# Performance work log

Measured on AMD Instinct MI355X. Metric: run time of the kernel, lower is better.

## Reference

```python
import jax, jax.numpy as jnp
import numpy as np

B, F, D = 1024, 39, 16
HIDDEN = [128, 128, 128]


def _cin(x, Ws, bs):
    # x: (B, F0, D) stacked field embeddings
    F0 = x.shape[1]
    h = x  # hidden_nn_layers[-1], shape (B, Fk, D)
    outs = []
    n = len(Ws)
    for i, (W, b) in enumerate(zip(Ws, bs)):
        L = W.shape[-1]
        Fk = h.shape[1]
        Wr = W.reshape(F0, Fk, L)  # conv1d kernel [1, F0*Fk, L] -> (F0, Fk, L)
        # per-embedding-dim field outer product: (B, F0, Fk, D)
        z = jnp.einsum('bfd,bgd->bfgd', x, h)
        # pointwise conv over D + bias + relu -> (B, L, D)
        cur = jax.nn.relu(jnp.einsum('bfgd,fgl->bld', z, Wr) + b[None, :, None])
        if i != n - 1:
            h = cur[:, : L // 2]          # next_hidden
            direct = cur[:, L // 2 :]     # direct_connect
        else:
            direct = cur
        outs.append(direct)
    # concat over field axis, sum over embedding dim -> (B, sum_direct)
    return jnp.concatenate(outs, axis=1).sum(-1)


def setup_inputs() -> dict:
    key = jax.random.key(0)
    ks = jax.random.split(key, 8)
    x = jax.random.normal(ks[0], (B, F, D), dtype=jnp.float32)
    field_nums = [F]
    Ws, bs = [], []
    for i, L in enumerate(HIDDEN):
        fan_in = field_nums[0] * field_nums[-1]
        lim = np.sqrt(6.0 / fan_in)  # he_uniform
        Ws.append(jax.random.uniform(ks[1 + i], (fan_in, L), jnp.float32, -lim, lim))
        bs.append(jnp.zeros((L,), jnp.float32))
        field_nums.append(L // 2)
    return {"x": x, "W0": Ws[0], "W1": Ws[1], "W2": Ws[2],
            "b0": bs[0], "b1": bs[1], "b2": bs[2]}


def reference(x, W0, W1, W2, b0, b1, b2):
    return _cin(x, [W0, W1, W2], [b0, b1, b2])
```

## Files before the change

kernel.cpp:

```cpp
#include <hip/hip_runtime.h>


#define NF     39
#define LCH    128
#define NLAYER 3
#define NFT    (NLAYER * NF)

typedef __bf16        bf16x8 __attribute__((ext_vector_type(8)));
typedef unsigned int  uint4v __attribute__((ext_vector_type(4)));
typedef float         f32x4  __attribute__((ext_vector_type(4)));

__device__ __forceinline__ unsigned short f2bf_rne(float f) {
    unsigned u = __float_as_uint(f);
    u += 0x7fffu + ((u >> 16) & 1u);
    return (unsigned short)(u >> 16);
}

__global__ void cin_prep(const float* __restrict__ W0,
                         const float* __restrict__ W1,
                         const float* __restrict__ W2,
                         unsigned short* __restrict__ wt)
{
    const int t = blockIdx.x * blockDim.x + threadIdx.x;
    if (t >= NFT * 1024) return;
    const int n  = t & 127;
    const int q  = (t >> 7) & 3;
    const int ks = (t >> 9) & 1;
    const int tl = t >> 10;
    const int l  = tl / NF;
    const int f  = tl - l * NF;
    const float* W = (l == 0) ? W0 : (l == 1) ? W1 : W2;

    unsigned short v[8];
    #pragma unroll
    for (int j = 0; j < 8; ++j) {
        const int g = ks * 32 + q * 8 + j;
        float w = 0.0f;
        if (l == 0) { if (g < NF) w = W[(f * NF + g) * LCH + n]; }
        else        { w = W[(f * 64 + g) * LCH + n]; }
        v[j] = f2bf_rne(w);
    }
    uint4v pv;
    #pragma unroll
    for (int i = 0; i < 4; ++i)
        pv[i] = (unsigned)v[2 * i] | ((unsigned)v[2 * i + 1] << 16);
    ((uint4v*)wt)[t] = pv;
}

__global__ __launch_bounds__(512, 2) void cin_mfma(
    const float* __restrict__ x,
    const unsigned short* __restrict__ wt,
    const float* __restrict__ b0p,
    const float* __restrict__ b1p,
    const float* __restrict__ b2p,
    float* __restrict__ out)
{
    __shared__ __align__(16) unsigned short hfrag[8 * 64 * 8];
    __shared__ float xf32[NF * 64];
    __shared__ float biasl[NLAYER * LCH];

    const int tid  = threadIdx.x;
    const int lane = tid & 63;
    const int w    = tid >> 6;
    const int q    = lane >> 4;
    const int c    = lane & 15;
    const int nc   = w * 16 + c;
    const int bb   = blockIdx.x * 4;

    {
        f32x4 z = {0.f, 0.f, 0.f, 0.f};
        ((f32x4*)hfrag)[tid] = z;
    }
    for (int t = tid; t < NLAYER * LCH; t += 512)
        biasl[t] = (t < 128) ? b0p[t] : (t < 256) ? b1p[t - 128] : b2p[t - 256];
    __syncthreads();

    for (int i = tid; i < 4 * NF * 16; i += 512) {
        const float v = x[bb * (NF * 16) + i];
        const int lb = i / (NF * 16);
        const int r  = i - lb * (NF * 16);
        const int f  = r >> 4;
        const int d  = r & 15;
        const int sl = lb * 16 + d;
        xf32[f * 64 + sl] = v;
        hfrag[((f >> 3) * 64 + sl) * 8 + (f & 7)] = f2bf_rne(v);
    }

    const unsigned short* wq = wt + (q * 128 + nc) * 8;

    bf16x8 c0 = *(const bf16x8*)(wq);
    bf16x8 c1 = *(const bf16x8*)(wq + 4096);
    bf16x8 n0 = *(const bf16x8*)(wq + 8192);
    bf16x8 n1 = *(const bf16x8*)(wq + 8192 + 4096);

    __syncthreads();

    #pragma unroll 1
    for (int l = 0; l < NLAYER; ++l) {
        bf16x8 a[2][4];
        #pragma unroll
        for (int ks = 0; ks < 2; ++ks)
            #pragma unroll
            for (int mt = 0; mt < 4; ++mt)
                a[ks][mt] = *(const bf16x8*)&hfrag[((ks * 4 + q) * 64 + mt * 16 + c) * 8];

        f32x4 cur[4];
        #pragma unroll
        for (int mt = 0; mt < 4; ++mt) cur[mt] = f32x4{0.f, 0.f, 0.f, 0.f};
        const f32x4 z = {0.f, 0.f, 0.f, 0.f};

        #pragma unroll 1
        for (int f = 0; f < NF; ++f) {
            const bf16x8 bv0 = c0;
            const bf16x8 bv1 = c1;

            #pragma unroll
            for (int mt = 0; mt < 4; ++mt) {
                f32x4 sv = __builtin_amdgcn_mfma_f32_16x16x32_bf16(a[0][mt], bv0, z,  0, 0, 0);
                sv       = __builtin_amdgcn_mfma_f32_16x16x32_bf16(a[1][mt], bv1, sv, 0, 0, 0);
                const f32x4 xr = *(const f32x4*)&xf32[f * 64 + mt * 16 + q * 4];
                #pragma unroll
                for (int r = 0; r < 4; ++r)
                    cur[mt][r] = fmaf(xr[r], sv[r], cur[mt][r]);
            }

            c0 = n0; c1 = n1;
            int pf = l * NF + f + 2; if (pf > NFT - 1) pf = NFT - 1;
            const unsigned short* p = wq + (size_t)pf * 8192;
            n0 = *(const bf16x8*)p;
            n1 = *(const bf16x8*)(p + 4096);
        }

        const float bias = biasl[l * LCH + nc];
        float v[4][4];
        #pragma unroll
        for (int mt = 0; mt < 4; ++mt)
            #pragma unroll
            for (int r = 0; r < 4; ++r)
                v[mt][r] = fmaxf(cur[mt][r] + bias, 0.f);

        if (l < 2 && w < 4) {
            #pragma unroll
            for (int mt = 0; mt < 4; ++mt)
                #pragma unroll
                for (int r = 0; r < 4; ++r)
                    hfrag[((nc >> 3) * 64 + mt * 16 + q * 4 + r) * 8 + (nc & 7)] =
                        f2bf_rne(v[mt][r]);
        } else {
            const int outcol = (l == 0) ? nc - 64 : (l == 1) ? nc : 128 + nc;
            #pragma unroll
            for (int mt = 0; mt < 4; ++mt) {
                float sacc = v[mt][0] + v[mt][1] + v[mt][2] + v[mt][3];
                sacc += __shfl_xor(sacc, 16, 64);
                sacc += __shfl_xor(sacc, 32, 64);
                if (lane < 16) out[(bb + mt) * 256 + outcol] = sacc;
            }
        }
        if (l < 2) __syncthreads();
    }
}

extern "C" void kernel_launch(void* const* d_in, const int* in_sizes, int n_in,
                              void* d_out, int out_size, void* d_ws, size_t ws_size,
                              hipStream_t stream) {
    const float* x  = (const float*)d_in[0];
    const float* W0 = (const float*)d_in[1];
    const float* W1 = (const float*)d_in[2];
    const float* W2 = (const float*)d_in[3];
    const float* b0 = (const float*)d_in[4];
    const float* b1 = (const float*)d_in[5];
    const float* b2 = (const float*)d_in[6];
    float* out = (float*)d_out;
    unsigned short* wt = (unsigned short*)d_ws;

    const int prep_threads = NFT * 1024;
    cin_prep<<<(prep_threads + 255) / 256, 256, 0, stream>>>(W0, W1, W2, wt);
    cin_mfma<<<256, 512, 0, stream>>>(x, wt, b0, b1, b2, out);
}
```

Baseline: 116.7 us.

## Halve batch rows per block, double grid, deepen weight prefetch

Each block now handles 2 batch rows instead of 4, so the grid doubles to 512 blocks and work spreads over more CUs on the 256-CU device. Launch bounds are raised to allow 4 blocks per CU. The weight prefetch pipeline is deepened from 2 to 3 stages and the field loop is unrolled by 3 to hide global load latency. The trade-off is that each weight fragment is now reused across only 2 M-tiles instead of 4, so global and L2 weight traffic per output doubles.

```diff
diff --git a/kernel.cpp b/kernel.cpp
--- a/kernel.cpp
+++ b/kernel.cpp
@@ -5,6 +5,9 @@
 #define LCH    128
 #define NLAYER 3
 #define NFT    (NLAYER * NF)
+#define BPB    2
+#define SL     (BPB * 16)
+#define MT     (SL / 16)
 
 typedef __bf16        bf16x8 __attribute__((ext_vector_type(8)));
 typedef unsigned int  uint4v __attribute__((ext_vector_type(4)));
@@ -47,7 +50,7 @@
     ((uint4v*)wt)[t] = pv;
 }
 
-__global__ __launch_bounds__(512, 2) void cin_mfma(
+__global__ __launch_bounds__(512, 4) void cin_mfma(
     const float* __restrict__ x,
     const unsigned short* __restrict__ wt,
     const float* __restrict__ b0p,
@@ -55,8 +58,8 @@
     const float* __restrict__ b2p,
     float* __restrict__ out)
 {
-    __shared__ __align__(16) unsigned short hfrag[8 * 64 * 8];
-    __shared__ float xf32[NF * 64];
+    __shared__ __align__(16) unsigned short hfrag[8 * SL * 8];
+    __shared__ float xf32[NF * SL];
     __shared__ float biasl[NLAYER * LCH];
 
     const int tid  = threadIdx.x;
@@ -65,91 +68,94 @@
     const int q    = lane >> 4;
     const int c    = lane & 15;
     const int nc   = w * 16 + c;
-    const int bb   = blockIdx.x * 4;
+    const int bb   = blockIdx.x * BPB;
 
     {
-        f32x4 z = {0.f, 0.f, 0.f, 0.f};
-        ((f32x4*)hfrag)[tid] = z;
+        f32x4 z4 = {0.f, 0.f, 0.f, 0.f};
+        if (tid < (8 * SL * 8) / 8) ((f32x4*)hfrag)[tid] = z4;
     }
     for (int t = tid; t < NLAYER * LCH; t += 512)
         biasl[t] = (t < 128) ? b0p[t] : (t < 256) ? b1p[t - 128] : b2p[t - 256];
     __syncthreads();
 
-    for (int i = tid; i < 4 * NF * 16; i += 512) {
+    for (int i = tid; i < BPB * NF * 16; i += 512) {
         const float v = x[bb * (NF * 16) + i];
         const int lb = i / (NF * 16);
         const int r  = i - lb * (NF * 16);
         const int f  = r >> 4;
         const int d  = r & 15;
         const int sl = lb * 16 + d;
-        xf32[f * 64 + sl] = v;
-        hfrag[((f >> 3) * 64 + sl) * 8 + (f & 7)] = f2bf_rne(v);
+        xf32[f * SL + sl] = v;
+        hfrag[((f >> 3) * SL + sl) * 8 + (f & 7)] = f2bf_rne(v);
     }
 
     const unsigned short* wq = wt + (q * 128 + nc) * 8;
 
     bf16x8 c0 = *(const bf16x8*)(wq);
     bf16x8 c1 = *(const bf16x8*)(wq + 4096);
-    bf16x8 n0 = *(const bf16x8*)(wq + 8192);
-    bf16x8 n1 = *(const bf16x8*)(wq + 8192 + 4096);
+    bf16x8 m0 = *(const bf16x8*)(wq + 8192);
+    bf16x8 m1 = *(const bf16x8*)(wq + 8192 + 4096);
+    bf16x8 n0 = *(const bf16x8*)(wq + 16384);
+    bf16x8 n1 = *(const bf16x8*)(wq + 16384 + 4096);
 
     __syncthreads();
 
     #pragma unroll 1
     for (int l = 0; l < NLAYER; ++l) {
-        bf16x8 a[2][4];
+        bf16x8 a[2][MT];
         #pragma unroll
         for (int ks = 0; ks < 2; ++ks)
             #pragma unroll
-            for (int mt = 0; mt < 4; ++mt)
-                a[ks][mt] = *(const bf16x8*)&hfrag[((ks * 4 + q) * 64 + mt * 16 + c) * 8];
+            for (int mt = 0; mt < MT; ++mt)
+                a[ks][mt] = *(const bf16x8*)&hfrag[((ks * 4 + q) * SL + mt * 16 + c) * 8];
 
-        f32x4 cur[4];
+        f32x4 cur[MT];
         #pragma unroll
-        for (int mt = 0; mt < 4; ++mt) cur[mt] = f32x4{0.f, 0.f, 0.f, 0.f};
+        for (int mt = 0; mt < MT; ++mt) cur[mt] = f32x4{0.f, 0.f, 0.f, 0.f};
         const f32x4 z = {0.f, 0.f, 0.f, 0.f};
 
-        #pragma unroll 1
+        #pragma unroll 3
         for (int f = 0; f < NF; ++f) {
             const bf16x8 bv0 = c0;
             const bf16x8 bv1 = c1;
 
             #pragma unroll
-            for (int mt = 0; mt < 4; ++mt) {
+            for (int mt = 0; mt < MT; ++mt) {
                 f32x4 sv = __builtin_amdgcn_mfma_f32_16x16x32_bf16(a[0][mt], bv0, z,  0, 0, 0);
                 sv       = __builtin_amdgcn_mfma_f32_16x16x32_bf16(a[1][mt], bv1, sv, 0, 0, 0);
-                const f32x4 xr = *(const f32x4*)&xf32[f * 64 + mt * 16 + q * 4];
+                const f32x4 xr = *(const f32x4*)&xf32[f * SL + mt * 16 + q * 4];
                 #pragma unroll
                 for (int r = 0; r < 4; ++r)
                     cur[mt][r] = fmaf(xr[r], sv[r], cur[mt][r]);
             }
 
-            c0 = n0; c1 = n1;
-            int pf = l * NF + f + 2; if (pf > NFT - 1) pf = NFT - 1;
+            c0 = m0; c1 = m1;
+            m0 = n0; m1 = n1;
+            int pf = l * NF + f + 3; if (pf > NFT - 1) pf = NFT - 1;
             const unsigned short* p = wq + (size_t)pf * 8192;
             n0 = *(const bf16x8*)p;
             n1 = *(const bf16x8*)(p + 4096);
         }
 
         const float bias = biasl[l * LCH + nc];
-        float v[4][4];
+        float v[MT][4];
         #pragma unroll
-        for (int mt = 0; mt < 4; ++mt)
+        for (int mt = 0; mt < MT; ++mt)
             #pragma unroll
             for (int r = 0; r < 4; ++r)
                 v[mt][r] = fmaxf(cur[mt][r] + bias, 0.f);
 
         if (l < 2 && w < 4) {
             #pragma unroll
-            for (int mt = 0; mt < 4; ++mt)
+            for (int mt = 0; mt < MT; ++mt)
                 #pragma unroll
                 for (int r = 0; r < 4; ++r)
-                    hfrag[((nc >> 3) * 64 + mt * 16 + q * 4 + r) * 8 + (nc & 7)] =
+                    hfrag[((nc >> 3) * SL + mt * 16 + q * 4 + r) * 8 + (nc & 7)] =
                         f2bf_rne(v[mt][r]);
         } else {
             const int outcol = (l == 0) ? nc - 64 : (l == 1) ? nc : 128 + nc;
             #pragma unroll
-            for (int mt = 0; mt < 4; ++mt) {
+            for (int mt = 0; mt < MT; ++mt) {
                 float sacc = v[mt][0] + v[mt][1] + v[mt][2] + v[mt][3];
                 sacc += __shfl_xor(sacc, 16, 64);
                 sacc += __shfl_xor(sacc, 32, 64);
@@ -175,5 +181,5 @@
 
     const int prep_threads = NFT * 1024;
     cin_prep<<<(prep_threads + 255) / 256, 256, 0, stream>>>(W0, W1, W2, wt);
-    cin_mfma<<<256, 512, 0, stream>>>(x, wt, b0, b1, b2, out);
+    cin_mfma<<<1024 / BPB, 512, 0, stream>>>(x, wt, b0, b1, b2, out);
 }
```

Result: faster. 107.5 us (-7.9%).

## Split field reduction across two wave groups and swap MFMA operand roles

Applied to the files above, without the earlier changes.

Doubles the block to 1024 threads. Each half of the waves handles half of the F0 field loop (padded to 40 so each half gets 20 zero-padded tiles), and the partial accumulators are combined through shared memory before bias and ReLU. It also swaps MFMA operands so weights are the A operand, relayouts the prepped weight tiles and the x buffer (transposed, padded) to fit, and deepens weight prefetch to four tiles. The aim is a shorter serial dependency chain per wave and more latency hiding, at the cost of an extra shared-memory reduction, a barrier, more registers per thread and a small amount of padded work.

```diff
diff --git a/kernel.cpp b/kernel.cpp
--- a/kernel.cpp
+++ b/kernel.cpp
@@ -1,10 +1,15 @@
 #include <hip/hip_runtime.h>
 
 
-#define NF     39
-#define LCH    128
-#define NLAYER 3
-#define NFT    (NLAYER * NF)
+#define NF      39
+#define LCH     128
+#define NLAYER  3
+#define LSTR    40
+#define NTILES  (NLAYER * LSTR)
+#define TILE_SH 8192
+#define SLN     64
+#define XPAD    44
+#define FHALF   20
 
 typedef __bf16        bf16x8 __attribute__((ext_vector_type(8)));
 typedef unsigned int  uint4v __attribute__((ext_vector_type(4)));
@@ -22,13 +27,13 @@
                          unsigned short* __restrict__ wt)
 {
     const int t = blockIdx.x * blockDim.x + threadIdx.x;
-    if (t >= NFT * 1024) return;
-    const int n  = t & 127;
-    const int q  = (t >> 7) & 3;
+    if (t >= NTILES * 1024) return;
+    const int q  = t & 3;
+    const int n  = (t >> 2) & 127;
     const int ks = (t >> 9) & 1;
     const int tl = t >> 10;
-    const int l  = tl / NF;
-    const int f  = tl - l * NF;
+    const int l  = tl / LSTR;
+    const int f  = tl - l * LSTR;
     const float* W = (l == 0) ? W0 : (l == 1) ? W1 : W2;
 
     unsigned short v[8];
@@ -36,8 +41,10 @@
     for (int j = 0; j < 8; ++j) {
         const int g = ks * 32 + q * 8 + j;
         float w = 0.0f;
-        if (l == 0) { if (g < NF) w = W[(f * NF + g) * LCH + n]; }
-        else        { w = W[(f * 64 + g) * LCH + n]; }
+        if (f < NF) {
+            if (l == 0) { if (g < NF) w = W[(f * NF + g) * LCH + n]; }
+            else        { w = W[(f * 64 + g) * LCH + n]; }
+        }
         v[j] = f2bf_rne(w);
     }
     uint4v pv;
@@ -47,7 +54,7 @@
     ((uint4v*)wt)[t] = pv;
 }
 
-__global__ __launch_bounds__(512, 2) void cin_mfma(
+__global__ __launch_bounds__(1024, 4) void cin_mfma(
     const float* __restrict__ x,
     const unsigned short* __restrict__ wt,
     const float* __restrict__ b0p,
@@ -55,105 +62,150 @@
     const float* __restrict__ b2p,
     float* __restrict__ out)
 {
-    __shared__ __align__(16) unsigned short hfrag[8 * 64 * 8];
-    __shared__ float xf32[NF * 64];
+    __shared__ __align__(16) unsigned short hfrag[8 * SLN * 8];
+    __shared__ __align__(16) float xT[SLN * XPAD];
     __shared__ float biasl[NLAYER * LCH];
+    __shared__ __align__(16) float rbuf[8 * 64 * 16];
 
     const int tid  = threadIdx.x;
     const int lane = tid & 63;
     const int w    = tid >> 6;
+    const int wn   = w & 7;
+    const int fh   = w >> 3;
     const int q    = lane >> 4;
     const int c    = lane & 15;
-    const int nc   = w * 16 + c;
+    const int nc   = wn * 16 + c;
     const int bb   = blockIdx.x * 4;
-
-    {
-        f32x4 z = {0.f, 0.f, 0.f, 0.f};
-        ((f32x4*)hfrag)[tid] = z;
-    }
-    for (int t = tid; t < NLAYER * LCH; t += 512)
-        biasl[t] = (t < 128) ? b0p[t] : (t < 256) ? b1p[t - 128] : b2p[t - 256];
+    const int fb   = fh * FHALF;
+
+    if (tid < 512) { f32x4 z4 = {0.f,0.f,0.f,0.f}; ((f32x4*)hfrag)[tid] = z4; }
+    if (tid < SLN) xT[tid * XPAD + NF] = 0.f;
+    if (tid < NLAYER * LCH)
+        biasl[tid] = (tid < 128) ? b0p[tid] : (tid < 256) ? b1p[tid-128] : b2p[tid-256];
     __syncthreads();
 
-    for (int i = tid; i < 4 * NF * 16; i += 512) {
+    for (int i = tid; i < 4 * NF * 16; i += 1024) {
         const float v = x[bb * (NF * 16) + i];
         const int lb = i / (NF * 16);
         const int r  = i - lb * (NF * 16);
         const int f  = r >> 4;
         const int d  = r & 15;
         const int sl = lb * 16 + d;
-        xf32[f * 64 + sl] = v;
-        hfrag[((f >> 3) * 64 + sl) * 8 + (f & 7)] = f2bf_rne(v);
+        xT[sl * XPAD + f] = v;
+        hfrag[((f >> 3) * SLN + sl) * 8 + (f & 7)] = f2bf_rne(v);
     }
-
-    const unsigned short* wq = wt + (q * 128 + nc) * 8;
-
-    bf16x8 c0 = *(const bf16x8*)(wq);
-    bf16x8 c1 = *(const bf16x8*)(wq + 4096);
-    bf16x8 n0 = *(const bf16x8*)(wq + 8192);
-    bf16x8 n1 = *(const bf16x8*)(wq + 8192 + 4096);
-
     __syncthreads();
+
+    const unsigned short* wqp = wt + (nc * 4 + q) * 8;
 
     #pragma unroll 1
     for (int l = 0; l < NLAYER; ++l) {
-        bf16x8 a[2][4];
+        bf16x8 h0[4], h1[4];
         #pragma unroll
-        for (int ks = 0; ks < 2; ++ks)
+        for (int st = 0; st < 4; ++st) {
+            h0[st] = *(const bf16x8*)&hfrag[(( q    ) * SLN + st * 16 + c) * 8];
+            h1[st] = *(const bf16x8*)&hfrag[((4 + q) * SLN + st * 16 + c) * 8];
+        }
+
+        const unsigned short* wl = wqp + (size_t)(l * LSTR + fb) * TILE_SH;
+        bf16x8 s0a = *(const bf16x8*)(wl);
+        bf16x8 s0b = *(const bf16x8*)(wl + 4096);
+        bf16x8 s1a = *(const bf16x8*)(wl + TILE_SH);
+        bf16x8 s1b = *(const bf16x8*)(wl + TILE_SH + 4096);
+        bf16x8 s2a = *(const bf16x8*)(wl + 2 * TILE_SH);
+        bf16x8 s2b = *(const bf16x8*)(wl + 2 * TILE_SH + 4096);
+        bf16x8 s3a = *(const bf16x8*)(wl + 3 * TILE_SH);
+        bf16x8 s3b = *(const bf16x8*)(wl + 3 * TILE_SH + 4096);
+
+        f32x4 cur0 = {0.f,0.f,0.f,0.f}, cur1 = cur0, cur2 = cur0, cur3 = cur0;
+        const f32x4 z = {0.f,0.f,0.f,0.f};
+
+        #pragma unroll 1
+        for (int fi4 = 0; fi4 < FHALF; fi4 += 4) {
+            const int xo = fb + fi4;
+            const f32x4 xq0 = *(const f32x4*)&xT[(0 * 16 + c) * XPAD + xo];
+            const f32x4 xq1 = *(const f32x4*)&xT[(1 * 16 + c) * XPAD + xo];
+            const f32x4 xq2 = *(const f32x4*)&xT[(2 * 16 + c) * XPAD + xo];
+            const f32x4 xq3 = *(const f32x4*)&xT[(3 * 16 + c) * XPAD + xo];
+
+#define SUBIT(J, SA, SB)                                                           \
+            {                                                                      \
+                f32x4 sv;                                                          \
+                sv = __builtin_amdgcn_mfma_f32_16x16x32_bf16(SA, h0[0], z, 0,0,0); \
+                sv = __builtin_amdgcn_mfma_f32_16x16x32_bf16(SB, h1[0], sv,0,0,0); \
+                cur0 += xq0[J] * sv;                                               \
+                sv = __builtin_amdgcn_mfma_f32_16x16x32_bf16(SA, h0[1], z, 0,0,0); \
+                sv = __builtin_amdgcn_mfma_f32_16x16x32_bf16(SB, h1[1], sv,0,0,0); \
+                cur1 += xq1[J] * sv;                                               \
+                sv = __builtin_amdgcn_mfma_f32_16x16x32_bf16(SA, h0[2], z, 0,0,0); \
+                sv = __builtin_amdgcn_mfma_f32_16x16x32_bf16(SB, h1[2], sv,0,0,0); \
+                cur2 += xq2[J] * sv;                                               \
+                sv = __builtin_amdgcn_mfma_f32_16x16x32_bf16(SA, h0[3], z, 0,0,0); \
+                sv = __builtin_amdgcn_mfma_f32_16x16x32_bf16(SB, h1[3], sv,0,0,0); \
+                cur3 += xq3[J] * sv;                                               \
+                int tn = l * LSTR + fb + fi4 + (J) + 4;                            \
+                if (tn > NTILES - 1) tn = NTILES - 1;                              \
+                const unsigned short* tp = wqp + (size_t)tn * TILE_SH;             \
+                SA = *(const bf16x8*)(tp);                                         \
+                SB = *(const bf16x8*)(tp + 4096);                                  \
+            }
+            SUBIT(0, s0a, s0b)
+            SUBIT(1, s1a, s1b)
+            SUBIT(2, s2a, s2b)
+            SUBIT(3, s3a, s3b)
+#undef SUBIT
+        }
+
+        if (fh == 1) {
+            float* rb = &rbuf[(wn * 64 + lane) * 16];
+            *(f32x4*)(rb +  0) = cur0;
+            *(f32x4*)(rb +  4) = cur1;
+            *(f32x4*)(rb +  8) = cur2;
+            *(f32x4*)(rb + 12) = cur3;
+        }
+        __syncthreads();
+        if (fh == 0) {
+            const float* rb = &rbuf[(wn * 64 + lane) * 16];
+            const f32x4 bq = *(const f32x4*)&biasl[l * LCH + wn * 16 + q * 4];
+            f32x4 vv0 = cur0 + *(const f32x4*)(rb +  0);
+            f32x4 vv1 = cur1 + *(const f32x4*)(rb +  4);
+            f32x4 vv2 = cur2 + *(const f32x4*)(rb +  8);
+            f32x4 vv3 = cur3 + *(const f32x4*)(rb + 12);
             #pragma unroll
-            for (int mt = 0; mt < 4; ++mt)
-                a[ks][mt] = *(const bf16x8*)&hfrag[((ks * 4 + q) * 64 + mt * 16 + c) * 8];
-
-        f32x4 cur[4];
-        #pragma unroll
-        for (int mt = 0; mt < 4; ++mt) cur[mt] = f32x4{0.f, 0.f, 0.f, 0.f};
-        const f32x4 z = {0.f, 0.f, 0.f, 0.f};
-
-        #pragma unroll 1
-        for (int f = 0; f < NF; ++f) {
-            const bf16x8 bv0 = c0;
-            const bf16x8 bv1 = c1;
-
-            #pragma unroll
-            for (int mt = 0; mt < 4; ++mt) {
-                f32x4 sv = __builtin_amdgcn_mfma_f32_16x16x32_bf16(a[0][mt], bv0, z,  0, 0, 0);
-                sv       = __builtin_amdgcn_mfma_f32_16x16x32_bf16(a[1][mt], bv1, sv, 0, 0, 0);
-                const f32x4 xr = *(const f32x4*)&xf32[f * 64 + mt * 16 + q * 4];
-                #pragma unroll
-                for (int r = 0; r < 4; ++r)
-                    cur[mt][r] = fmaf(xr[r], sv[r], cur[mt][r]);
+            for (int r = 0; r < 4; ++r) {
+                vv0[r] = fmaxf(vv0[r] + bq[r], 0.f);
+                vv1[r] = fmaxf(vv1[r] + bq[r], 0.f);
+                vv2[r] = fmaxf(vv2[r] + bq[r], 0.f);
+                vv3[r] = fmaxf(vv3[r] + bq[r], 0.f);
             }
-
-            c0 = n0; c1 = n1;
-            int pf = l * NF + f + 2; if (pf > NFT - 1) pf = NFT - 1;
-            const unsigned short* p = wq + (size_t)pf * 8192;
-            n0 = *(const bf16x8*)p;
-            n1 = *(const bf16x8*)(p + 4096);
-        }
-
-        const float bias = biasl[l * LCH + nc];
-        float v[4][4];
-        #pragma unroll
-        for (int mt = 0; mt < 4; ++mt)
-            #pragma unroll
-            for (int r = 0; r < 4; ++r)
-                v[mt][r] = fmaxf(cur[mt][r] + bias, 0.f);
-
-        if (l < 2 && w < 4) {
-            #pragma unroll
-            for (int mt = 0; mt < 4; ++mt)
-                #pragma unroll
-                for (int r = 0; r < 4; ++r)
-                    hfrag[((nc >> 3) * 64 + mt * 16 + q * 4 + r) * 8 + (nc & 7)] =
-                        f2bf_rne(v[mt][r]);
-        } else {
-            const int outcol = (l == 0) ? nc - 64 : (l == 1) ? nc : 128 + nc;
-            #pragma unroll
-            for (int mt = 0; mt < 4; ++mt) {
-                float sacc = v[mt][0] + v[mt][1] + v[mt][2] + v[mt][3];
-                sacc += __shfl_xor(sacc, 16, 64);
-                sacc += __shfl_xor(sacc, 32, 64);
-                if (lane < 16) out[(bb + mt) * 256 + outcol] = sacc;
+            if (l < 2 && wn < 4) {
+#define HWR(ST, VV)                                                            \
+                _Pragma("unroll")                                              \
+                for (int r = 0; r < 4; ++r) {                                  \
+                    const int n = wn * 16 + q * 4 + r;                         \
+                    hfrag[((n >> 3) * SLN + (ST) * 16 + c) * 8 + (n & 7)] =    \
+                        f2bf_rne(VV[r]);                                       \
+                }
+                HWR(0, vv0) HWR(1, vv1) HWR(2, vv2) HWR(3, vv3)
+#undef HWR
+            } else {
+#define DST(ST, VV)                                                            \
+                _Pragma("unroll")                                              \
+                for (int r = 0; r < 4; ++r) {                                  \
+                    float s = VV[r];                                           \
+                    s += __shfl_xor(s, 1, 64);                                 \
+                    s += __shfl_xor(s, 2, 64);                                 \
+                    s += __shfl_xor(s, 4, 64);                                 \
+                    s += __shfl_xor(s, 8, 64);                                 \
+                    if (c == 0) {                                              \
+                        const int n = wn * 16 + q * 4 + r;                     \
+                        const int outcol = (l == 0) ? n - 64                   \
+                                         : (l == 1) ? n : 128 + n;             \
+                        out[(bb + (ST)) * 256 + outcol] = s;                   \
+                    }                                                          \
+                }
+                DST(0, vv0) DST(1, vv1) DST(2, vv2) DST(3, vv3)
+#undef DST
             }
         }
         if (l < 2) __syncthreads();
@@ -173,7 +225,7 @@
     float* out = (float*)d_out;
     unsigned short* wt = (unsigned short*)d_ws;
 
-    const int prep_threads = NFT * 1024;
+    const int prep_threads = NTILES * 1024;
     cin_prep<<<(prep_threads + 255) / 256, 256, 0, stream>>>(W0, W1, W2, wt);
-    cin_mfma<<<256, 512, 0, stream>>>(x, wt, b0, b1, b2, out);
-}
+    cin_mfma<<<256, 1024, 0, stream>>>(x, wt, b0, b1, b2, out);
+}
```

Result: faster. 110.1 us (-5.6%).

## Stage weight tiles in LDS via async loads and split K across waves

Applied to the files above, without the earlier changes.

Weight tiles are now staged into double-buffered shared memory with global_load_lds in phases of three fields, replacing per-thread register prefetch from global memory. Block size doubles to 1024 threads, and the two K-halves of the MFMA are split across wave groups, with partial sums reduced through a shared buffer. The x values are read directly from global memory with a register prefetch instead of an LDS copy. The aim is to hide weight load latency and raise MFMA parallelism per CU, at the cost of a block barrier every phase and an extra reduction step per layer.

```diff
diff --git a/kernel.cpp b/kernel.cpp
--- a/kernel.cpp
+++ b/kernel.cpp
@@ -1,10 +1,15 @@
 #include <hip/hip_runtime.h>
 
 
-#define NF     39
-#define LCH    128
-#define NLAYER 3
-#define NFT    (NLAYER * NF)
+#define NF      39
+#define LCH     128
+#define NLAYER  3
+#define NFT     (NLAYER * NF)
+#define TILE_SH 8192
+#define PH_T    3
+#define BUF_SH  (PH_T * TILE_SH)
+#define SLN     64
+#define NPH     (NF / PH_T)
 
 typedef __bf16        bf16x8 __attribute__((ext_vector_type(8)));
 typedef unsigned int  uint4v __attribute__((ext_vector_type(4)));
@@ -47,7 +52,7 @@
     ((uint4v*)wt)[t] = pv;
 }
 
-__global__ __launch_bounds__(512, 2) void cin_mfma(
+__global__ __launch_bounds__(1024, 4) void cin_mfma(
     const float* __restrict__ x,
     const unsigned short* __restrict__ wt,
     const float* __restrict__ b0p,
@@ -55,105 +60,150 @@
     const float* __restrict__ b2p,
     float* __restrict__ out)
 {
-    __shared__ __align__(16) unsigned short hfrag[8 * 64 * 8];
-    __shared__ float xf32[NF * 64];
-    __shared__ float biasl[NLAYER * LCH];
+    __shared__ __align__(16) unsigned short Bbuf[2 * BUF_SH];
+    __shared__ __align__(16) unsigned short hfrag[8 * SLN * 8];
+    __shared__ __align__(16) float rbuf[16 * 512];
 
     const int tid  = threadIdx.x;
     const int lane = tid & 63;
     const int w    = tid >> 6;
+    const int wn   = w & 7;
+    const int ksh  = w >> 3;
     const int q    = lane >> 4;
     const int c    = lane & 15;
-    const int nc   = w * 16 + c;
+    const int nc   = wn * 16 + c;
     const int bb   = blockIdx.x * 4;
 
-    {
-        f32x4 z = {0.f, 0.f, 0.f, 0.f};
-        ((f32x4*)hfrag)[tid] = z;
-    }
-    for (int t = tid; t < NLAYER * LCH; t += 512)
-        biasl[t] = (t < 128) ? b0p[t] : (t < 256) ? b1p[t - 128] : b2p[t - 256];
+    if (tid < 512) {
+        f32x4 z4 = {0.f, 0.f, 0.f, 0.f};
+        ((f32x4*)hfrag)[tid] = z4;
+    }
     __syncthreads();
 
-    for (int i = tid; i < 4 * NF * 16; i += 512) {
+    for (int i = tid; i < 4 * NF * 16; i += 1024) {
         const float v = x[bb * (NF * 16) + i];
         const int lb = i / (NF * 16);
         const int r  = i - lb * (NF * 16);
         const int f  = r >> 4;
         const int d  = r & 15;
         const int sl = lb * 16 + d;
-        xf32[f * 64 + sl] = v;
-        hfrag[((f >> 3) * 64 + sl) * 8 + (f & 7)] = f2bf_rne(v);
-    }
-
-    const unsigned short* wq = wt + (q * 128 + nc) * 8;
-
-    bf16x8 c0 = *(const bf16x8*)(wq);
-    bf16x8 c1 = *(const bf16x8*)(wq + 4096);
-    bf16x8 n0 = *(const bf16x8*)(wq + 8192);
-    bf16x8 n1 = *(const bf16x8*)(wq + 8192 + 4096);
+        hfrag[((f >> 3) * SLN + sl) * 8 + (f & 7)] = f2bf_rne(v);
+    }
+
+    {
+        const unsigned short* src = wt + w * 512 + lane * 8;
+        unsigned short* dst = Bbuf + w * 512;
+        #pragma unroll
+        for (int k = 0; k < PH_T; ++k)
+            __builtin_amdgcn_global_load_lds((const void*)(src + k * TILE_SH),
+                                             (void*)(dst + k * TILE_SH), 16, 0, 0);
+    }
+
+    const float* xb = x + bb * (NF * 16) + q * 4;
 
     __syncthreads();
 
+    int cb = 0;
     #pragma unroll 1
     for (int l = 0; l < NLAYER; ++l) {
-        bf16x8 a[2][4];
-        #pragma unroll
-        for (int ks = 0; ks < 2; ++ks)
+        bf16x8 a[4];
+        #pragma unroll
+        for (int mt = 0; mt < 4; ++mt)
+            a[mt] = *(const bf16x8*)&hfrag[((ksh * 4 + q) * SLN + mt * 16 + c) * 8];
+
+        f32x4 cur[4];
+        #pragma unroll
+        for (int mt = 0; mt < 4; ++mt) cur[mt] = f32x4{0.f, 0.f, 0.f, 0.f};
+        const f32x4 zz = {0.f, 0.f, 0.f, 0.f};
+
+        f32x4 xc[4], xn[4];
+        #pragma unroll
+        for (int mt = 0; mt < 4; ++mt) {
+            xc[mt] = *(const f32x4*)(xb + mt * (NF * 16));
+            xn[mt] = *(const f32x4*)(xb + mt * (NF * 16) + 16);
+        }
+
+        #pragma unroll 1
+        for (int ph = 0; ph < NPH; ++ph) {
+            const int tl = l * NF + ph * PH_T;
+
+            const int nb = tl + PH_T;
+            if (nb < NFT) {
+                const unsigned short* src = wt + (size_t)nb * TILE_SH + w * 512 + lane * 8;
+                unsigned short* dst = &Bbuf[(cb ^ 1) * BUF_SH + w * 512];
+                #pragma unroll
+                for (int k = 0; k < PH_T; ++k)
+                    __builtin_amdgcn_global_load_lds((const void*)(src + k * TILE_SH),
+                                                     (void*)(dst + k * TILE_SH), 16, 0, 0);
+            }
+
+            const unsigned short* rbq = Bbuf + cb * BUF_SH + ((ksh * 4 + q) * 128 + nc) * 8;
+            const bf16x8 B0 = *(const bf16x8*)(rbq);
+            const bf16x8 B1 = *(const bf16x8*)(rbq + TILE_SH);
+            const bf16x8 B2 = *(const bf16x8*)(rbq + 2 * TILE_SH);
+
+            #define F_ITER(BK, FI)                                                  \
+            {                                                                       \
+                _Pragma("unroll")                                                   \
+                for (int mt = 0; mt < 4; ++mt) {                                    \
+                    const f32x4 sv = __builtin_amdgcn_mfma_f32_16x16x32_bf16(       \
+                        a[mt], BK, zz, 0, 0, 0);                                    \
+                    _Pragma("unroll")                                               \
+                    for (int r = 0; r < 4; ++r)                                     \
+                        cur[mt][r] = fmaf(xc[mt][r], sv[r], cur[mt][r]);            \
+                }                                                                   \
+                int fn = (FI) + 2; if (fn > NF - 1) fn = NF - 1;                    \
+                _Pragma("unroll")                                                   \
+                for (int mt = 0; mt < 4; ++mt) {                                    \
+                    xc[mt] = xn[mt];                                                \
+                    xn[mt] = *(const f32x4*)(xb + mt * (NF * 16) + fn * 16);        \
+                }                                                                   \
+            }
+            F_ITER(B0, ph * PH_T + 0)
+            F_ITER(B1, ph * PH_T + 1)
+            F_ITER(B2, ph * PH_T + 2)
+            #undef F_ITER
+
+            __syncthreads();
+            cb ^= 1;
+        }
+
+        if (ksh == 1) {
             #pragma unroll
             for (int mt = 0; mt < 4; ++mt)
-                a[ks][mt] = *(const bf16x8*)&hfrag[((ks * 4 + q) * 64 + mt * 16 + c) * 8];
-
-        f32x4 cur[4];
-        #pragma unroll
-        for (int mt = 0; mt < 4; ++mt) cur[mt] = f32x4{0.f, 0.f, 0.f, 0.f};
-        const f32x4 z = {0.f, 0.f, 0.f, 0.f};
-
-        #pragma unroll 1
-        for (int f = 0; f < NF; ++f) {
-            const bf16x8 bv0 = c0;
-            const bf16x8 bv1 = c1;
-
-            #pragma unroll
-            for (int mt = 0; mt < 4; ++mt) {
-                f32x4 sv = __builtin_amdgcn_mfma_f32_16x16x32_bf16(a[0][mt], bv0, z,  0, 0, 0);
-                sv       = __builtin_amdgcn_mfma_f32_16x16x32_bf16(a[1][mt], bv1, sv, 0, 0, 0);
-                const f32x4 xr = *(const f32x4*)&xf32[f * 64 + mt * 16 + q * 4];
                 #pragma unroll
                 for (int r = 0; r < 4; ++r)
-                    cur[mt][r] = fmaf(xr[r], sv[r], cur[mt][r]);
-            }
-
-            c0 = n0; c1 = n1;
-            int pf = l * NF + f + 2; if (pf > NFT - 1) pf = NFT - 1;
-            const unsigned short* p = wq + (size_t)pf * 8192;
-            n0 = *(const bf16x8*)p;
-            n1 = *(const bf16x8*)(p + 4096);
-        }
-
-        const float bias = biasl[l * LCH + nc];
-        float v[4][4];
-        #pragma unroll
-        for (int mt = 0; mt < 4; ++mt)
-            #pragma unroll
-            for (int r = 0; r < 4; ++r)
-                v[mt][r] = fmaxf(cur[mt][r] + bias, 0.f);
-
-        if (l < 2 && w < 4) {
+                    rbuf[(mt * 4 + r) * 512 + wn * 64 + lane] = cur[mt][r];
+        }
+        __syncthreads();
+        if (ksh == 0) {
+            const float* bp = (l == 0) ? b0p : (l == 1) ? b1p : b2p;
+            const float bias = bp[nc];
+            float v[4][4];
             #pragma unroll
             for (int mt = 0; mt < 4; ++mt)
                 #pragma unroll
                 for (int r = 0; r < 4; ++r)
-                    hfrag[((nc >> 3) * 64 + mt * 16 + q * 4 + r) * 8 + (nc & 7)] =
-                        f2bf_rne(v[mt][r]);
-        } else {
-            const int outcol = (l == 0) ? nc - 64 : (l == 1) ? nc : 128 + nc;
-            #pragma unroll
-            for (int mt = 0; mt < 4; ++mt) {
-                float sacc = v[mt][0] + v[mt][1] + v[mt][2] + v[mt][3];
-                sacc += __shfl_xor(sacc, 16, 64);
-                sacc += __shfl_xor(sacc, 32, 64);
-                if (lane < 16) out[(bb + mt) * 256 + outcol] = sacc;
+                    v[mt][r] = fmaxf(cur[mt][r] +
+                                     rbuf[(mt * 4 + r) * 512 + wn * 64 + lane] +
+                                     bias, 0.f);
+
+            if (l < 2 && wn < 4) {
+                #pragma unroll
+                for (int mt = 0; mt < 4; ++mt)
+                    #pragma unroll
+                    for (int r = 0; r < 4; ++r)
+                        hfrag[((nc >> 3) * SLN + mt * 16 + q * 4 + r) * 8 + (nc & 7)] =
+                            f2bf_rne(v[mt][r]);
+            } else {
+                const int outcol = (l == 0) ? nc - 64 : (l == 1) ? nc : 128 + nc;
+                #pragma unroll
+                for (int mt = 0; mt < 4; ++mt) {
+                    float sacc = v[mt][0] + v[mt][1] + v[mt][2] + v[mt][3];
+                    sacc += __shfl_xor(sacc, 16, 64);
+                    sacc += __shfl_xor(sacc, 32, 64);
+                    if (lane < 16) out[(bb + mt) * 256 + outcol] = sacc;
+                }
             }
         }
         if (l < 2) __syncthreads();
@@ -175,5 +225,5 @@
 
     const int prep_threads = NFT * 1024;
     cin_prep<<<(prep_threads + 255) / 256, 256, 0, stream>>>(W0, W1, W2, wt);
-    cin_mfma<<<256, 512, 0, stream>>>(x, wt, b0, b1, b2, out);
-}
+    cin_mfma<<<256, 1024, 0, stream>>>(x, wt, b0, b1, b2, out);
+}
```

Measured after the change: 184.5 us. 58.1% more time.
